# Kernel tuning notes

Measured on AMD Instinct MI355X. Metric: run time of the kernel, lower is better.

## Reference

```python
import jax, jax.numpy as jnp
import numpy as np

B, S, D, H, E, K = 4, 1024, 1024, 4096, 8, 2
CAPACITY_FACTOR = 2.0
T = B * S
CAP = int(T * CAPACITY_FACTOR * K / E)  # 2048


def setup_inputs() -> dict:
    key = jax.random.key(0)
    ks = jax.random.split(key, 6)
    std = 0.02
    return {
        "x": jax.random.normal(ks[0], (B, S, D), dtype=jnp.float32),
        "router_w": jax.random.normal(ks[1], (E, D), dtype=jnp.float32) * std,
        "w1": jax.random.normal(ks[2], (E, D, H), dtype=jnp.float32) * std,
        "b1": jnp.zeros((E, H), dtype=jnp.float32),
        "w2": jax.random.normal(ks[3], (E, H, D), dtype=jnp.float32) * std,
        "b2": jnp.zeros((E, D), dtype=jnp.float32),
    }


def reference(x, router_w, w1, b1, w2, b2):
    # Router (eval mode: no logit noise, no dropout)
    logits = jnp.einsum("bsd,ed->bse", x, router_w)            # [B,S,E]
    probs = jax.nn.softmax(logits, axis=-1)
    topk_p, topk_i = jax.lax.top_k(probs, K)                   # [B,S,K]
    gates = topk_p / jnp.sum(topk_p, axis=-1, keepdims=True)

    xt = x.reshape(T, D)                                        # tokens
    eidx = topk_i.reshape(T * K)                                # expert per slot
    g = gates.reshape(T * K)
    tok = jnp.arange(T * K) // K                                # token id per slot

    # position of each slot within its expert (first-come-first-served capacity)
    oh = jax.nn.one_hot(eidx, E, dtype=jnp.int32)               # [T*K, E]
    pos = jnp.sum((jnp.cumsum(oh, axis=0) - 1) * oh, axis=1)    # [T*K]
    keep = pos < CAP
    pos_c = jnp.where(keep, pos, CAP)                           # overflow -> padding row

    # dispatch: gather tokens into per-expert buffers [E, CAP, D]
    buf = jnp.zeros((E, CAP + 1, D), x.dtype).at[eidx, pos_c].set(xt[tok])
    inp = buf[:, :CAP]

    # per-expert FFN (exact-erf GELU matches torch nn.GELU default)
    h = jax.nn.gelu(jnp.einsum("ecd,edh->ech", inp, w1) + b1[:, None, :],
                    approximate=False)
    out_e = jnp.einsum("ech,eho->eco", h, w2) + b2[:, None, :]  # [E,CAP,D]

    # combine: gather back to slots, weight by gates, sum over k per token
    gathered = out_e[eidx, jnp.minimum(pos_c, CAP - 1)]         # [T*K, D]
    wslot = g * keep.astype(x.dtype)
    out = (gathered * wslot[:, None]).reshape(T, K, D).sum(axis=1).reshape(B, S, D)

    # load-balancing loss
    router_prob_per_expert = probs.mean(axis=(0, 1))            # [E]
    expert_usage = oh.sum(axis=0).astype(x.dtype) / (T * K)
    lb_loss = jnp.sum(router_prob_per_expert * expert_usage) * E
    return out, lb_loss
```

## Files before the change

kernel.cpp:

```cpp
#include <hip/hip_runtime.h>
#include <cstdint>
#include <cstddef>

#define TDIM 4096
#define DDIM 1024
#define HDIM 4096
#define EDIM 8
#define CAPD 2048
#define NSLOT 8192
#define NROUTERBLK 1024

typedef _Float16 f16;
typedef _Float16 f16x2 __attribute__((ext_vector_type(2)));
typedef _Float16 f16x4 __attribute__((ext_vector_type(4)));
typedef _Float16 f16x8 __attribute__((ext_vector_type(8)));
typedef float f32x4 __attribute__((ext_vector_type(4)));

__device__ __forceinline__ void gload16(const void* g, void* l) {
  __builtin_amdgcn_global_load_lds(
      (const __attribute__((address_space(1))) unsigned int*)g,
      (__attribute__((address_space(3))) unsigned int*)l, 16, 0, 0);
}

__device__ __forceinline__ float gelu_fast(float x) {
  float y = 1.5957691216057308f * (x + 0.044715f * x * x * x);
  y = fminf(y, 60.f);
  float e = __expf(y);
  return x * e * __builtin_amdgcn_rcpf(e + 1.f);
}

#define MEMFENCE asm volatile("" ::: "memory")

__global__ __launch_bounds__(256)
void transpose_cvt(const float* __restrict__ src, f16* __restrict__ dst, int R, int C) {
  __shared__ float tile[64][65];
  const int e = blockIdx.z;
  const int c0 = blockIdx.x * 64, r0 = blockIdx.y * 64;
  const int tid = threadIdx.x;
  const float* s = src + (size_t)e * R * C;
  f16* d = dst + (size_t)e * R * C;
  #pragma unroll
  for (int p = 0; p < 4; ++p) {
    const int row = p * 16 + (tid >> 4);
    const int col = (tid & 15) * 4;
    float4 v = *(const float4*)(s + (size_t)(r0 + row) * C + c0 + col);
    tile[row][col] = v.x; tile[row][col + 1] = v.y;
    tile[row][col + 2] = v.z; tile[row][col + 3] = v.w;
  }
  __syncthreads();
  #pragma unroll
  for (int p = 0; p < 4; ++p) {
    const int crow = p * 16 + (tid >> 4);
    const int q = (tid & 15) * 4;
    f16x4 o;
    #pragma unroll
    for (int j = 0; j < 4; ++j) o[j] = (f16)tile[q + j][crow];
    *(f16x4*)(d + (size_t)(c0 + crow) * R + r0 + q) = o;
  }
}

__global__ void router_k(const float* __restrict__ x, const float* __restrict__ rw,
                         int* __restrict__ eidx, float* __restrict__ gates,
                         float* __restrict__ bps) {
  __shared__ float lrw[EDIM * DDIM];
  __shared__ float wps[4][EDIM];
  const int tid = threadIdx.x, lane = tid & 63, wv = tid >> 6;
  for (int i = tid; i < EDIM * DDIM; i += 256) lrw[i] = rw[i];
  __syncthreads();
  const int t = blockIdx.x * 4 + wv;
  float acc[EDIM];
  #pragma unroll
  for (int e = 0; e < EDIM; ++e) acc[e] = 0.f;
  const float* xr = x + (size_t)t * DDIM;
  #pragma unroll
  for (int j = 0; j < DDIM / 64; ++j) {
    float xv = xr[j * 64 + lane];
    #pragma unroll
    for (int e = 0; e < EDIM; ++e) acc[e] += xv * lrw[e * DDIM + j * 64 + lane];
  }
  #pragma unroll
  for (int off = 32; off >= 1; off >>= 1) {
    #pragma unroll
    for (int e = 0; e < EDIM; ++e) acc[e] += __shfl_xor(acc[e], off);
  }
  float mx = acc[0];
  #pragma unroll
  for (int e = 1; e < EDIM; ++e) mx = fmaxf(mx, acc[e]);
  float p[EDIM], s = 0.f;
  #pragma unroll
  for (int e = 0; e < EDIM; ++e) { p[e] = expf(acc[e] - mx); s += p[e]; }
  float inv = 1.f / s;
  #pragma unroll
  for (int e = 0; e < EDIM; ++e) p[e] *= inv;
  int i1 = 0; float p1 = p[0];
  #pragma unroll
  for (int e = 1; e < EDIM; ++e) if (p[e] > p1) { p1 = p[e]; i1 = e; }
  int i2 = (i1 == 0) ? 1 : 0; float p2 = p[i2];
  #pragma unroll
  for (int e = 0; e < EDIM; ++e) if (e != i1 && p[e] > p2) { p2 = p[e]; i2 = e; }
  float gs = 1.f / (p1 + p2);
  if (lane == 0) {
    eidx[2 * t] = i1; eidx[2 * t + 1] = i2;
    gates[2 * t] = p1 * gs; gates[2 * t + 1] = p2 * gs;
    #pragma unroll
    for (int e = 0; e < EDIM; ++e) wps[wv][e] = p[e];
  }
  __syncthreads();
  if (tid < EDIM)
    bps[blockIdx.x * EDIM + tid] = wps[0][tid] + wps[1][tid] + wps[2][tid] + wps[3][tid];
}

__global__ void count_k(const int* __restrict__ eidx, int* __restrict__ cc) {
  __shared__ int h[EDIM];
  const int tid = threadIdx.x;
  if (tid < EDIM) h[tid] = 0;
  __syncthreads();
  atomicAdd(&h[eidx[blockIdx.x * 256 + tid]], 1);
  __syncthreads();
  if (tid < EDIM) cc[blockIdx.x * EDIM + tid] = h[tid];
}

__global__ void scan_k(const int* __restrict__ cc, const float* __restrict__ bps,
                       int* __restrict__ cb, int* __restrict__ counts,
                       int* __restrict__ rowsNeeded, float* __restrict__ lb_out) {
  __shared__ float red[32][EDIM];
  __shared__ int cnt_s[EDIM];
  const int tid = threadIdx.x;
  const int e = tid & 7, g = tid >> 3;
  float s = 0.f;
  for (int j = 0; j < 32; ++j) s += bps[(g + 32 * j) * EDIM + e];
  red[g][e] = s;
  __syncthreads();
  for (int st = 16; st >= 1; st >>= 1) {
    if (g < st) red[g][e] += red[g + st][e];
    __syncthreads();
  }
  if (tid < EDIM) {
    int base = 0;
    for (int c = 0; c < 32; ++c) { cb[c * EDIM + tid] = base; base += cc[c * EDIM + tid]; }
    counts[tid] = base;
    rowsNeeded[tid] = base < CAPD ? base : CAPD;
    cnt_s[tid] = base;
  }
  __syncthreads();
  if (tid == 0) {
    float lb = 0.f;
    for (int ee = 0; ee < EDIM; ++ee)
      lb += (red[0][ee] / (float)TDIM) * ((float)cnt_s[ee] / (float)NSLOT);
    lb_out[0] = lb * (float)EDIM;
  }
}

__global__ void pos_k(const int* __restrict__ eidx, const float* __restrict__ gates,
                      const int* __restrict__ cb, int* __restrict__ posa,
                      float* __restrict__ wslot) {
  __shared__ int wcnt[4][EDIM];
  const int tid = threadIdx.x, lane = tid & 63, wv = tid >> 6;
  const int slot = blockIdx.x * 256 + tid;
  const int e = eidx[slot];
  const unsigned long long below = (1ull << lane) - 1ull;
  int wavepos = 0;
  #pragma unroll
  for (int ee = 0; ee < EDIM; ++ee) {
    unsigned long long m = __ballot(e == ee);
    if (lane == 0) wcnt[wv][ee] = __popcll(m);
    if (e == ee) wavepos = __popcll(m & below);
  }
  __syncthreads();
  int off = 0;
  for (int w = 0; w < wv; ++w) off += wcnt[w][e];
  const int pos = cb[blockIdx.x * EDIM + e] + off + wavepos;
  posa[slot] = pos;
  wslot[slot] = (pos < CAPD) ? gates[slot] : 0.f;
}

__global__ void scatter_k(const float* __restrict__ x, const int* __restrict__ eidx,
                          const int* __restrict__ posa, f16* __restrict__ buf) {
  const int s = blockIdx.x, lane = threadIdx.x;
  const int p = posa[s];
  if (p >= CAPD) return;
  const int e = eidx[s], tok = s >> 1;
  const float4* src = (const float4*)(x + (size_t)tok * DDIM);
  f16x4* dst = (f16x4*)(buf + ((size_t)e * CAPD + p) * DDIM);
  #pragma unroll
  for (int j = 0; j < DDIM / 4 / 64; ++j) {
    float4 v = src[j * 64 + lane];
    f16x4 o; o.x = (f16)v.x; o.y = (f16)v.y; o.z = (f16)v.z; o.w = (f16)v.w;
    dst[j * 64 + lane] = o;
  }
}

#define STAGE(bb, hh, g) do { \
    const f16* s_ = sP[hh] + (g) * 64; \
    char* d_ = smem + (bb) * 32768 + (hh) * 8192 + wv * 1024; \
    gload16(s_, d_); \
    gload16(s_ + (size_t)32 * LD, d_ + 4096); \
  } while (0)

template<int KLEN, int LD, int N, int GELU, int NT, int NKS>
__global__ __launch_bounds__(256, 2)
void gemm128(const f16* __restrict__ A, const f16* __restrict__ Bt,
             const float* __restrict__ bias, f16* __restrict__ C, size_t pstride,
             const int* __restrict__ rowsNeeded) {
  constexpr int NTT = KLEN / 64;
  __shared__ __align__(128) char smem[65536];
  const int wg = blockIdx.x;
  const int e = wg & 7;
  const int r = wg >> 3;
  const int nt = r % NT;
  const int ks = (r / NT) % NKS;
  const int mt = r / (NT * NKS);
  if (mt * 128 >= rowsNeeded[e]) return;
  const int tid = threadIdx.x, lane = tid & 63, wv = tid >> 6;
  const int wr = wv >> 1, wc = wv & 1;
  const int ro = lane & 15, q4 = (lane >> 4) * 4;
  const int ko0b = (lane >> 4) * 16;
  const f16* aBase = A + ((size_t)e * CAPD + (size_t)mt * 128) * LD + (size_t)ks * KLEN;
  const f16* bBase = Bt + ((size_t)e * N + (size_t)nt * 128) * LD + (size_t)ks * KLEN;
  const int row0 = tid >> 3;
  const int sw0 = ((tid & 7) ^ (row0 & 7)) * 8;

  const f16* sP[4];
  sP[0] = aBase + (size_t)row0 * LD + sw0;
  sP[1] = sP[0] + (size_t)64 * LD;
  sP[2] = bBase + (size_t)row0 * LD + sw0;
  sP[3] = sP[2] + (size_t)64 * LD;

  int aoffs[4][2], boffs[4][2];
  #pragma unroll
  for (int m = 0; m < 4; ++m)
    #pragma unroll
    for (int k = 0; k < 2; ++k) {
      const int rh = wr * 64 + m * 16 + ro;
      aoffs[m][k] = rh * 128 + ((k * 64 + ko0b) ^ ((rh & 7) << 4));
      const int rb = wc * 64 + m * 16 + ro;
      boffs[m][k] = 16384 + rb * 128 + ((k * 64 + ko0b) ^ ((rb & 7) << 4));
    }

  f32x4 acc[4][4];
  #pragma unroll
  for (int m = 0; m < 4; ++m)
    #pragma unroll
    for (int n = 0; n < 4; ++n) acc[m][n] = (f32x4){0.f, 0.f, 0.f, 0.f};

  STAGE(0, 0, 0); STAGE(0, 1, 0); STAGE(0, 2, 0); STAGE(0, 3, 0);
  asm volatile("s_waitcnt vmcnt(0)" ::: "memory");
  __builtin_amdgcn_sched_barrier(0);
  __builtin_amdgcn_s_barrier(); MEMFENCE;

  #pragma unroll 1
  for (int t = 0; t < NTT; ++t) {
    const int cb = (t & 1) << 15;
    if (t + 1 < NTT) {
      const int ab = (t & 1) ^ 1;
      STAGE(ab, 0, t + 1); STAGE(ab, 1, t + 1);
      STAGE(ab, 2, t + 1); STAGE(ab, 3, t + 1);
    }
    f16x8 af[4][2], bf[4][2];
    #pragma unroll
    for (int m = 0; m < 4; ++m)
      #pragma unroll
      for (int k = 0; k < 2; ++k) {
        af[m][k] = *(const f16x8*)(smem + cb + aoffs[m][k]);
        bf[m][k] = *(const f16x8*)(smem + cb + boffs[m][k]);
      }
    #pragma unroll
    for (int k = 0; k < 2; ++k)
      #pragma unroll
      for (int m = 0; m < 4; ++m)
        #pragma unroll
        for (int n = 0; n < 4; ++n)
          acc[m][n] = __builtin_amdgcn_mfma_f32_16x16x32_f16(af[m][k], bf[n][k], acc[m][n], 0, 0, 0);
    asm volatile("s_waitcnt lgkmcnt(0)" ::: "memory");
    asm volatile("s_waitcnt vmcnt(0)" ::: "memory");
    __builtin_amdgcn_sched_barrier(0);
    __builtin_amdgcn_s_barrier(); MEMFENCE;
  }

  float bv[4];
  #pragma unroll
  for (int n = 0; n < 4; ++n)
    bv[n] = (ks == 0) ? bias[e * N + nt * 128 + wc * 64 + n * 16 + ro] : 0.f;
  f16* Ct = (f16*)(smem + wv * 8192);
  #pragma unroll
  for (int m = 0; m < 4; ++m)
    #pragma unroll
    for (int n = 0; n < 4; ++n)
      #pragma unroll
      for (int i = 0; i < 4; ++i) {
        const int row = m * 16 + q4 + i;
        float v = acc[m][n][i] + bv[n];
        if (GELU) v = gelu_fast(v);
        *(f16*)((char*)Ct + row * 128 + (((n * 16 + ro) * 2) ^ (((row >> 2) & 3) << 5))) = (f16)v;
      }
  asm volatile("s_waitcnt lgkmcnt(0)" ::: "memory");
  __builtin_amdgcn_sched_barrier(0);
  f16* Cp = C + (size_t)ks * pstride;
  const size_t crow0 = (size_t)e * CAPD + mt * 128 + wr * 64;
  const int ccol0 = nt * 128 + wc * 64;
  #pragma unroll
  for (int j = 0; j < 8; ++j) {
    const int idx = j * 64 + lane;
    const int rr = idx >> 3, c2 = (idx & 7) * 16;
    f16x8 v = *(const f16x8*)((const char*)Ct + rr * 128 + (c2 ^ (((rr >> 2) & 3) << 5)));
    *(f16x8*)(Cp + (crow0 + rr) * N + ccol0 + (idx & 7) * 8) = v;
  }
}

__global__ void combine_k(const f16* __restrict__ pA, const f16* __restrict__ pB,
                          const int* __restrict__ eidx, const int* __restrict__ posa,
                          const float* __restrict__ wslot, float* __restrict__ out) {
  const int t = blockIdx.x, tid = threadIdx.x;
  const int s0 = 2 * t, s1 = 2 * t + 1;
  const int e0 = eidx[s0], e1 = eidx[s1];
  int p0 = posa[s0]; p0 = p0 < CAPD - 1 ? p0 : CAPD - 1;
  int p1 = posa[s1]; p1 = p1 < CAPD - 1 ? p1 : CAPD - 1;
  const float g0 = wslot[s0], g1 = wslot[s1];
  const size_t o0 = ((size_t)e0 * CAPD + p0) * DDIM;
  const size_t o1 = ((size_t)e1 * CAPD + p1) * DDIM;
  const f16x2* r0a = (const f16x2*)(pA + o0);
  const f16x2* r0b = (const f16x2*)(pB + o0);
  const f16x2* r1a = (const f16x2*)(pA + o1);
  const f16x2* r1b = (const f16x2*)(pB + o1);
  float2* o = (float2*)(out + (size_t)t * DDIM);
  #pragma unroll
  for (int j = tid; j < DDIM / 2; j += 256) {
    f16x2 a0 = r0a[j], a1 = r0b[j], b0 = r1a[j], b1 = r1b[j];
    o[j] = make_float2(
        g0 * ((float)a0.x + (float)a1.x) + g1 * ((float)b0.x + (float)b1.x),
        g0 * ((float)a0.y + (float)a1.y) + g1 * ((float)b0.y + (float)b1.y));
  }
}

extern "C" void kernel_launch(void* const* d_in, const int* in_sizes, int n_in,
                              void* d_out, int out_size, void* d_ws, size_t ws_size,
                              hipStream_t stream) {
  (void)in_sizes; (void)n_in; (void)out_size; (void)ws_size;
  const float* x  = (const float*)d_in[0];
  const float* rw = (const float*)d_in[1];
  const float* w1 = (const float*)d_in[2];
  const float* b1 = (const float*)d_in[3];
  const float* w2 = (const float*)d_in[4];
  const float* b2 = (const float*)d_in[5];
  float* out = (float*)d_out;

  char* ws = (char*)d_ws;
  size_t off = 0;
  auto alloc = [&](size_t b) { void* p = ws + off; off += (b + 255) & ~(size_t)255; return p; };
  f16* w1t   = (f16*)alloc((size_t)EDIM * DDIM * HDIM * 2);
  f16* w2t   = (f16*)alloc((size_t)EDIM * DDIM * HDIM * 2);
  f16* buf   = (f16*)alloc((size_t)EDIM * CAPD * DDIM * 2);
  f16* hbuf  = (f16*)alloc((size_t)EDIM * CAPD * HDIM * 2);
  const size_t PSTRIDE = (size_t)EDIM * CAPD * DDIM;
  f16* outeA = (f16*)alloc(PSTRIDE * 2);
  f16* outeB = (f16*)alloc(PSTRIDE * 2);
  int*   eidx   = (int*)alloc(NSLOT * 4);
  int*   posa   = (int*)alloc(NSLOT * 4);
  float* gatesA = (float*)alloc(NSLOT * 4);
  float* wslotA = (float*)alloc(NSLOT * 4);
  int*   cc     = (int*)alloc(32 * EDIM * 4);
  int*   cb     = (int*)alloc(32 * EDIM * 4);
  int*   counts = (int*)alloc(EDIM * 4);
  int*   rowsN  = (int*)alloc(EDIM * 4);
  float* bps    = (float*)alloc(NROUTERBLK * EDIM * 4);
  (void)outeB;

  transpose_cvt<<<dim3(HDIM / 64, DDIM / 64, EDIM), 256, 0, stream>>>(w1, w1t, DDIM, HDIM);
  transpose_cvt<<<dim3(DDIM / 64, HDIM / 64, EDIM), 256, 0, stream>>>(w2, w2t, HDIM, DDIM);

  router_k<<<NROUTERBLK, 256, 0, stream>>>(x, rw, eidx, gatesA, bps);
  count_k<<<32, 256, 0, stream>>>(eidx, cc);
  scan_k<<<1, 256, 0, stream>>>(cc, bps, cb, counts, rowsN, out + (size_t)TDIM * DDIM);
  pos_k<<<32, 256, 0, stream>>>(eidx, gatesA, cb, posa, wslotA);
  scatter_k<<<NSLOT, 64, 0, stream>>>(x, eidx, posa, buf);

  gemm128<DDIM, DDIM, HDIM, 1, 32, 1><<<4096, 256, 0, stream>>>(
      buf, w1t, b1, hbuf, 0, rowsN);

  gemm128<HDIM / 2, HDIM, DDIM, 0, 8, 2><<<2048, 256, 0, stream>>>(
      hbuf, w2t, b2, outeA, PSTRIDE, rowsN);

  combine_k<<<TDIM, 256, 0, stream>>>(outeA, outeA + PSTRIDE, eidx, posa, wslotA, out);
}
```

Before: 318.5 us.

## Replace double-buffered GEMM staging with single buffer for higher occupancy

The expert GEMM kernel drops its double-buffered LDS pipeline (64KB) for a single 32KB buffer. Each k-step now loads the tile, syncs, computes, and syncs again. Launch bounds go from 2 to 4 blocks per CU, so that occupancy can hide memory latency in place of explicit prefetch overlap. The cost is losing overlap of global loads with MFMA inside a block, and each block now pays the load latency on every iteration.

Measured after the change: 300.8 us. -5.6%, faster.

```diff
diff --git a/kernel.cpp b/kernel.cpp
--- a/kernel.cpp
+++ b/kernel.cpp
@@ -28,8 +28,6 @@
   float e = __expf(y);
   return x * e * __builtin_amdgcn_rcpf(e + 1.f);
 }
-
-#define MEMFENCE asm volatile("" ::: "memory")
 
 __global__ __launch_bounds__(256)
 void transpose_cvt(const float* __restrict__ src, f16* __restrict__ dst, int R, int C) {
@@ -190,20 +188,20 @@
   }
 }
 
-#define STAGE(bb, hh, g) do { \
+#define STAGE(hh, g) do { \
     const f16* s_ = sP[hh] + (g) * 64; \
-    char* d_ = smem + (bb) * 32768 + (hh) * 8192 + wv * 1024; \
+    char* d_ = smem + (hh) * 8192 + wv * 1024; \
     gload16(s_, d_); \
     gload16(s_ + (size_t)32 * LD, d_ + 4096); \
   } while (0)
 
 template<int KLEN, int LD, int N, int GELU, int NT, int NKS>
-__global__ __launch_bounds__(256, 2)
-void gemm128(const f16* __restrict__ A, const f16* __restrict__ Bt,
-             const float* __restrict__ bias, f16* __restrict__ C, size_t pstride,
-             const int* __restrict__ rowsNeeded) {
+__global__ __launch_bounds__(256, 4)
+void gemm128s(const f16* __restrict__ A, const f16* __restrict__ Bt,
+              const float* __restrict__ bias, f16* __restrict__ C, size_t pstride,
+              const int* __restrict__ rowsNeeded) {
   constexpr int NTT = KLEN / 64;
-  __shared__ __align__(128) char smem[65536];
+  __shared__ __align__(128) char smem[32768];
   const int wg = blockIdx.x;
   const int e = wg & 7;
   const int r = wg >> 3;
@@ -243,26 +241,17 @@
     #pragma unroll
     for (int n = 0; n < 4; ++n) acc[m][n] = (f32x4){0.f, 0.f, 0.f, 0.f};
 
-  STAGE(0, 0, 0); STAGE(0, 1, 0); STAGE(0, 2, 0); STAGE(0, 3, 0);
-  asm volatile("s_waitcnt vmcnt(0)" ::: "memory");
-  __builtin_amdgcn_sched_barrier(0);
-  __builtin_amdgcn_s_barrier(); MEMFENCE;
-
   #pragma unroll 1
   for (int t = 0; t < NTT; ++t) {
-    const int cb = (t & 1) << 15;
-    if (t + 1 < NTT) {
-      const int ab = (t & 1) ^ 1;
-      STAGE(ab, 0, t + 1); STAGE(ab, 1, t + 1);
-      STAGE(ab, 2, t + 1); STAGE(ab, 3, t + 1);
-    }
+    STAGE(0, t); STAGE(1, t); STAGE(2, t); STAGE(3, t);
+    __syncthreads();
     f16x8 af[4][2], bf[4][2];
     #pragma unroll
     for (int m = 0; m < 4; ++m)
       #pragma unroll
       for (int k = 0; k < 2; ++k) {
-        af[m][k] = *(const f16x8*)(smem + cb + aoffs[m][k]);
-        bf[m][k] = *(const f16x8*)(smem + cb + boffs[m][k]);
+        af[m][k] = *(const f16x8*)(smem + aoffs[m][k]);
+        bf[m][k] = *(const f16x8*)(smem + boffs[m][k]);
       }
     #pragma unroll
     for (int k = 0; k < 2; ++k)
@@ -271,10 +260,7 @@
         #pragma unroll
         for (int n = 0; n < 4; ++n)
           acc[m][n] = __builtin_amdgcn_mfma_f32_16x16x32_f16(af[m][k], bf[n][k], acc[m][n], 0, 0, 0);
-    asm volatile("s_waitcnt lgkmcnt(0)" ::: "memory");
-    asm volatile("s_waitcnt vmcnt(0)" ::: "memory");
-    __builtin_amdgcn_sched_barrier(0);
-    __builtin_amdgcn_s_barrier(); MEMFENCE;
+    __syncthreads();
   }
 
   float bv[4];
@@ -374,10 +360,10 @@
   pos_k<<<32, 256, 0, stream>>>(eidx, gatesA, cb, posa, wslotA);
   scatter_k<<<NSLOT, 64, 0, stream>>>(x, eidx, posa, buf);
 
-  gemm128<DDIM, DDIM, HDIM, 1, 32, 1><<<4096, 256, 0, stream>>>(
+  gemm128s<DDIM, DDIM, HDIM, 1, 32, 1><<<4096, 256, 0, stream>>>(
       buf, w1t, b1, hbuf, 0, rowsN);
 
-  gemm128<HDIM / 2, HDIM, DDIM, 0, 8, 2><<<2048, 256, 0, stream>>>(
+  gemm128s<HDIM / 2, HDIM, DDIM, 0, 8, 2><<<2048, 256, 0, stream>>>(
       hbuf, w2t, b2, outeA, PSTRIDE, rowsN);
 
   combine_k<<<TDIM, 256, 0, stream>>>(outeA, outeA + PSTRIDE, eidx, posa, wslotA, out);
```
